# Performance work log

Measured on AMD Instinct MI355X. Metric: run time of the kernel, lower is better.

The kernel has to match this reference:

```python
import jax, jax.numpy as jnp
import numpy as np

B, L, D, H, K = 8, 2048, 1024, 16, 31
D_CONV = D // H  # 64
EPS = 1e-6


def setup_inputs() -> dict:
    key = jax.random.key(0)
    ks = jax.random.split(key, 5)
    return {
        "x": jax.random.normal(ks[0], (B, L, D), dtype=jnp.float32),
        "W_pe": (jax.random.normal(ks[1], (D_CONV, 2 * K), dtype=jnp.float32) * 0.1),
        "b_pe": jnp.zeros((2 * K,), dtype=jnp.float32),
        "stt_energy": jnp.ones((1, H, 1, K), dtype=jnp.float32)
                      + 0.02 * jax.random.normal(ks[2], (1, H, 1, K), dtype=jnp.float32),
        "W_fc": jax.random.normal(ks[3], (D, D), dtype=jnp.float32) / jnp.sqrt(jnp.float32(D)),
        "gamma": jnp.ones((D,), dtype=jnp.float32),
        "beta": jnp.zeros((D,), dtype=jnp.float32),
    }


def reference(x, W_pe, b_pe, stt_energy, W_fc, gamma, beta):
    b, l, d_model = x.shape
    d = d_model // H
    residual = x

    # mask_table matmul == causal running mean: avg[t] = mean(x[0..t])
    avg = jnp.cumsum(x, axis=1) / jnp.arange(1, l + 1, dtype=x.dtype)[None, :, None]

    # (B, L, H, d) -> (B*H, L, d)
    ci = avg.reshape(b, l, H, d).transpose(0, 2, 1, 3).reshape(b * H, l, d)

    pc = ci @ W_pe + b_pe                      # (BH, L, 2K)
    dyn, gate = pc[..., :K], pc[..., K:]
    stt = jnp.broadcast_to(stt_energy, (b, H, 1, K)).reshape(b * H, 1, K)
    energy = stt + jax.nn.sigmoid(gate) * dyn  # (BH, L, K)

    # as_strided banded softmax: energy[t,k] attends position t+k-(K-1);
    # -10000 fillers underflow to 0 in fp32, and out-of-range (negative position)
    # weights are dropped WITHOUT renormalization, as in the original slicing.
    w = jax.nn.softmax(energy, axis=-1)        # (BH, L, K)
    t_idx = jnp.arange(l)[:, None]
    k_idx = jnp.arange(K)[None, :]
    w = jnp.where(t_idx + k_idx - (K - 1) >= 0, w, jnp.zeros((), x.dtype))

    # banded bmm: out[t] = sum_k w[t,k] * ci[t+k-(K-1)]
    padded = jnp.pad(ci, ((0, 0), (K - 1, 0), (0, 0)))  # (BH, L+K-1, d)
    out = jnp.zeros((b * H, l, d), dtype=x.dtype)
    for kk in range(K):  # small fixed kernel-size loop
        out = out + w[:, :, kk:kk + 1] * padded[:, kk:kk + l, :]

    conv_loc = out.reshape(b, H, l, d).transpose(0, 2, 1, 3).reshape(b, l, d_model)

    v = conv_loc @ W_fc.T + residual
    mu = jnp.mean(v, axis=-1, keepdims=True)
    var = jnp.var(v, axis=-1, keepdims=True)
    v = (v - mu) / jnp.sqrt(var + EPS) * gamma + beta
    return v
```

## Files before the change

kernel.cpp:

```cpp
#include <hip/hip_runtime.h>
#include <math.h>

#define BB 8
#define LL 2048
#define DD 1024
#define HH 16
#define DH 64
#define KK 31
#define NSEG 32
#define SEGLEN 64

#define TLEN 64
#define TROW 2080
#define TSTR2 112
#define WBSTR2 104
#define WPESTR2 72
#define PCSS 64

typedef __attribute__((ext_vector_type(8))) short bf16x8;
typedef __attribute__((ext_vector_type(4))) float f32x4;
typedef __attribute__((ext_vector_type(8))) unsigned short u16x8;

__device__ __forceinline__ unsigned short f2bf(float f) {
    unsigned u = __float_as_uint(f);
    unsigned r = (u + 0x7fffu + ((u >> 16) & 1u)) >> 16;
    return (unsigned short)r;
}
__device__ __forceinline__ float bf2f(unsigned short s) {
    return __uint_as_float(((unsigned)s) << 16);
}

__device__ __forceinline__ void gload_lds16(const void* g, void* l) {
    __builtin_amdgcn_global_load_lds(
        (const __attribute__((address_space(1))) void*)g,
        (__attribute__((address_space(3))) void*)l, 16, 0, 0);
}

__global__ __launch_bounds__(256)
void seg_sum_kernel(const float* __restrict__ x, float* __restrict__ segsum) {
    int g = blockIdx.x * 256 + threadIdx.x;
    int d = g & (DD - 1);
    int s = (g >> 10) & (NSEG - 1);
    int b = g >> 15;
    const float* p = x + (size_t)(b * LL + s * SEGLEN) * DD + d;
    float acc = 0.f;
    #pragma unroll 8
    for (int i = 0; i < SEGLEN; ++i) acc += p[(size_t)i * DD];
    segsum[g] = acc;
}

__global__ __launch_bounds__(256)
void avg_kernel(const float* __restrict__ x, const float* __restrict__ segsum,
                unsigned short* __restrict__ avgT) {
    int g = blockIdx.x * 256 + threadIdx.x;
    int d = g & (DD - 1);
    int s = (g >> 10) & (NSEG - 1);
    int b = g >> 15;
    float run = 0.f;
    const float* ss = segsum + ((size_t)b << 15) + d;
    for (int s2 = 0; s2 < s; ++s2) run += ss[s2 << 10];
    const float* p = x + (size_t)(b * LL + s * SEGLEN) * DD + d;
    unsigned short* rowt = avgT +
        ((size_t)(b * HH + (d >> 6)) * DH + (d & 63)) * TROW;
    unsigned short* qt = rowt + 32 + s * SEGLEN;
    if (s == 0) {
        u16x8 z = {};
        #pragma unroll
        for (int j = 0; j < 4; ++j) *(u16x8*)&rowt[j * 8] = z;
    }
    int t0 = s * SEGLEN;
    #pragma unroll
    for (int j = 0; j < 8; ++j) {
        u16x8 v;
        #pragma unroll
        for (int e = 0; e < 8; ++e) {
            int i = j * 8 + e;
            run += p[(size_t)i * DD];
            v[e] = f2bf(run / (float)(t0 + i + 1));
        }
        *(u16x8*)&qt[j * 8] = v;
    }
}

__global__ __launch_bounds__(256, 4)
void conv_kernel(const unsigned short* __restrict__ avgT,
                 const unsigned short* __restrict__ wpeT,
                 const float* __restrict__ b_pe, const float* __restrict__ stt,
                 unsigned short* __restrict__ conv) {
    __shared__ __align__(16) unsigned short pcs[64 * PCSS];
    __shared__ __align__(16) unsigned short winT[64 * TSTR2];
    __shared__ __align__(16) unsigned short wub[64 * WBSTR2];

    int tid = threadIdx.x;
    int tile = blockIdx.x & 31;
    int bh = blockIdx.x >> 5;
    int b = bh >> 4, h = bh & 15;
    int t0 = tile * TLEN;
    int wv = tid >> 6, ln = tid & 63;
    int g = ln >> 4, li = ln & 15;

    {
        const unsigned short* gT = avgT + (size_t)(b * HH + h) * DH * TROW;
        #pragma unroll
        for (int q = 0; q < 3; ++q) {
            int i = tid + q * 256;
            int d = i / 14, c = i - d * 14;
            gload_lds16(gT + (size_t)d * TROW + t0 + c * 8, winT + (i & ~63) * 8);
        }
        if (tid < 128) {
            int i = 768 + tid;
            int d = i / 14, c = i - d * 14;
            gload_lds16(gT + (size_t)d * TROW + t0 + c * 8, winT + (i & ~63) * 8);
        }
        #pragma unroll
        for (int q = 0; q < 2; ++q) {
            int i = tid + q * 256;
            gload_lds16(wpeT + i * 8, wub + (i & ~63) * 8);
        }
        if (tid < 64) {
            int i = 512 + tid;
            gload_lds16(wpeT + i * 8, wub + (i & ~63) * 8);
        }
    }
    __syncthreads();

    f32x4 pacc[4];
    {
        int q32 = 32 + wv * 16 + li;
        bf16x8 a0, a1;
        #pragma unroll
        for (int e = 0; e < 8; ++e) {
            a0[e] = (short)winT[(g * 8 + e) * TSTR2 + q32];
            a1[e] = (short)winT[(32 + g * 8 + e) * TSTR2 + q32];
        }
        #pragma unroll
        for (int n = 0; n < 4; ++n) {
            int c = n * 16 + li;
            bf16x8 b0 = *(const bf16x8*)&wub[c * WPESTR2 + g * 8];
            bf16x8 b1 = *(const bf16x8*)&wub[c * WPESTR2 + 32 + g * 8];
            f32x4 z = {0.f, 0.f, 0.f, 0.f};
            z = __builtin_amdgcn_mfma_f32_16x16x32_bf16(a0, b0, z, 0, 0, 0);
            z = __builtin_amdgcn_mfma_f32_16x16x32_bf16(a1, b1, z, 0, 0, 0);
            pacc[n] = z;
        }
    }
    __syncthreads();

    {
        #pragma unroll
        for (int n = 0; n < 4; ++n) {
            int c = n * 16 + li;
            float bp = (c < 2 * KK) ? b_pe[c] : 0.f;
            #pragma unroll
            for (int r = 0; r < 4; ++r)
                pcs[(wv * 16 + g * 4 + r) * PCSS + c] = f2bf(pacc[n][r] + bp);
        }
        for (int i = tid; i < 64 * WBSTR2 / 8; i += 256) {
            u16x8 z = {};
            *(u16x8*)&wub[i * 8] = z;
        }
    }
    __syncthreads();

    {
        int half = ln >> 5, k = ln & 31;
        int kc = (k < KK) ? k : 0;
        float sttk = stt[h * KK + kc];
        for (int it = 0; it < 8; ++it) {
            int tok = wv * 16 + it * 2 + half;
            float dyn  = bf2f(pcs[tok * PCSS + kc]);
            float gate = bf2f(pcs[tok * PCSS + KK + kc]);
            float e = 0.f;
            if (k < KK) e = __expf(sttk + dyn / (1.f + __expf(-gate)));
            float sum = e;
            #pragma unroll
            for (int off = 16; off; off >>= 1) sum += __shfl_xor(sum, off, 64);
            float wvl = e / sum;
            if (k < KK && t0 + tok + k >= KK - 1)
                wub[tok * WBSTR2 + tok + k + 2] = f2bf(wvl);
        }
    }
    __syncthreads();

    {
        int row = wv * 16 + li;
        bf16x8 wa0 = *(const bf16x8*)&wub[row * WBSTR2 + g * 8];
        bf16x8 wa1 = *(const bf16x8*)&wub[row * WBSTR2 + 32 + g * 8];
        bf16x8 wa2 = *(const bf16x8*)&wub[row * WBSTR2 + 64 + g * 8];
        f32x4 cacc[4];
        #pragma unroll
        for (int n = 0; n < 4; ++n) {
            int c = n * 16 + li;
            bf16x8 b0 = *(const bf16x8*)&winT[c * TSTR2 + g * 8];
            bf16x8 b1 = *(const bf16x8*)&winT[c * TSTR2 + 32 + g * 8];
            bf16x8 b2 = *(const bf16x8*)&winT[c * TSTR2 + 64 + g * 8];
            f32x4 z = {0.f, 0.f, 0.f, 0.f};
            z = __builtin_amdgcn_mfma_f32_16x16x32_bf16(wa0, b0, z, 0, 0, 0);
            z = __builtin_amdgcn_mfma_f32_16x16x32_bf16(wa1, b1, z, 0, 0, 0);
            z = __builtin_amdgcn_mfma_f32_16x16x32_bf16(wa2, b2, z, 0, 0, 0);
            cacc[n] = z;
        }
        #pragma unroll
        for (int n = 0; n < 4; ++n)
            #pragma unroll
            for (int r = 0; r < 4; ++r)
                pcs[(wv * 16 + g * 4 + r) * PCSS + n * 16 + li] =
                    f2bf(cacc[n][r]);
    }
    __syncthreads();

    {
        int tok = tid >> 2, j0 = (tid & 3) * 16;
        u16x8 v0 = *(const u16x8*)&pcs[tok * PCSS + j0];
        u16x8 v1 = *(const u16x8*)&pcs[tok * PCSS + j0 + 8];
        unsigned short* o = conv + (size_t)(b * LL + t0 + tok) * DD + h * DH + j0;
        *(u16x8*)&o[0] = v0;
        *(u16x8*)&o[8] = v1;
    }
}

__global__ __launch_bounds__(256)
void cvt_kernel(const float* __restrict__ in, unsigned short* __restrict__ out,
                const float* __restrict__ W_pe, unsigned short* __restrict__ wpeT) {
    if (blockIdx.x == 1024) {
        for (int i = threadIdx.x; i < 64 * WPESTR2; i += 256) {
            int c = i / WPESTR2, d = i - c * WPESTR2;
            float v = (c < 2 * KK && d < 64) ? W_pe[d * (2 * KK) + c] : 0.f;
            wpeT[i] = f2bf(v);
        }
        return;
    }
    int i = (blockIdx.x * 256 + threadIdx.x) * 4;
    float4 v = *(const float4*)&in[i];
    ushort4 o;
    o.x = f2bf(v.x); o.y = f2bf(v.y); o.z = f2bf(v.z); o.w = f2bf(v.w);
    *(ushort4*)&out[i] = o;
}

#define WAITV2() do { asm volatile("s_waitcnt vmcnt(2)" ::: "memory"); \
                      __builtin_amdgcn_sched_barrier(0); } while (0)
#define WAITV0() do { asm volatile("s_waitcnt vmcnt(0)" ::: "memory"); \
                      __builtin_amdgcn_sched_barrier(0); } while (0)
#define BAR()    do { __builtin_amdgcn_s_barrier(); \
                      __builtin_amdgcn_sched_barrier(0); } while (0)

__global__ __launch_bounds__(512, 2)
void gemm_mfma_kernel(const unsigned short* __restrict__ A,
                      const unsigned short* __restrict__ Bt,
                      const float* __restrict__ X,
                      unsigned short* __restrict__ Vb)
{
    __shared__ __align__(16) unsigned short As0[256 * 64];
    __shared__ __align__(16) unsigned short Bs0[256 * 64];
    __shared__ __align__(16) unsigned short As1[256 * 64];
    __shared__ __align__(16) unsigned short Bs1[256 * 64];
    int tid = threadIdx.x;
    int wv = tid >> 6, ln = tid & 63;
    int bid = blockIdx.x;
    int nbid = (bid & 7) * 32 + (bid >> 3);
    int bm0 = (nbid >> 2) * 256;
    int bn0 = (nbid & 3) * 256;
    int wr = wv >> 2, wc = wv & 3;

    const unsigned short* ga[4];
    const unsigned short* gb[4];
    int ldo[4];
    #pragma unroll
    for (int i = 0; i < 4; ++i) {
        int dci = i * 512 + wv * 64 + ln;
        int row = dci >> 3, ch = dci & 7;
        int sc = ch ^ (row & 7);
        ga[i] = A  + (size_t)(bm0 + row) * 1024 + sc * 8;
        gb[i] = Bt + (size_t)(bn0 + row) * 1024 + sc * 8;
        ldo[i] = dci * 8;
    }

    f32x4 acc[8][4] = {};
    int la = wr * 128 + (ln & 15);
    int lb = wc * 64 + (ln & 15);
    int kg = ln >> 4;

#define TILE(RA, RB, SA, SB, ktn, LAST)                                       \
  {                                                                           \
    if (!(LAST)) { gload_lds16(ga[0] + (ktn), SA + ldo[0]);                   \
                   gload_lds16(ga[1] + (ktn), SA + ldo[1]); }                 \
    if (LAST) { WAITV0(); } else { WAITV2(); }                                \
    BAR();                                                                    \
    bf16x8 bfr[4][2];                                                         \
    _Pragma("unroll")                                                         \
    for (int n = 0; n < 4; ++n)                                               \
      _Pragma("unroll")                                                       \
      for (int ks = 0; ks < 2; ++ks) {                                        \
        int row = lb + n * 16;                                                \
        bfr[n][ks] = *(const bf16x8*)&RB[row * 64 +                           \
                        (((kg + ks * 4) ^ (row & 7)) * 8)];                   \
      }                                                                       \
    _Pragma("unroll")                                                         \
    for (int mq = 0; mq < 4; ++mq) {                                          \
      if (!(LAST)) {                                                          \
        if (mq == 1) { gload_lds16(ga[2] + (ktn), SA + ldo[2]);               \
                       gload_lds16(ga[3] + (ktn), SA + ldo[3]); }             \
        if (mq == 2) { gload_lds16(gb[0] + (ktn), SB + ldo[0]);               \
                       gload_lds16(gb[1] + (ktn), SB + ldo[1]); }             \
        if (mq == 3) { gload_lds16(gb[2] + (ktn), SB + ldo[2]);               \
                       gload_lds16(gb[3] + (ktn), SB + ldo[3]); }             \
      }                                                                       \
      bf16x8 af[2][2];                                                        \
      _Pragma("unroll")                                                       \
      for (int mm = 0; mm < 2; ++mm)                                          \
        _Pragma("unroll")                                                     \
        for (int ks = 0; ks < 2; ++ks) {                                      \
          int row = la + (mq * 2 + mm) * 16;                                  \
          af[mm][ks] = *(const bf16x8*)&RA[row * 64 +                         \
                          (((kg + ks * 4) ^ (row & 7)) * 8)];                 \
        }                                                                     \
      __builtin_amdgcn_s_setprio(1);                                          \
      _Pragma("unroll")                                                       \
      for (int mm = 0; mm < 2; ++mm)                                          \
        _Pragma("unroll")                                                     \
        for (int n = 0; n < 4; ++n)                                           \
          _Pragma("unroll")                                                   \
          for (int ks = 0; ks < 2; ++ks)                                      \
            acc[mq * 2 + mm][n] = __builtin_amdgcn_mfma_f32_16x16x32_bf16(    \
                af[mm][ks], bfr[n][ks], acc[mq * 2 + mm][n], 0, 0, 0);        \
      __builtin_amdgcn_s_setprio(0);                                          \
    }                                                                         \
    BAR();                                                                    \
  }

    #pragma unroll
    for (int i = 0; i < 4; ++i) {
        gload_lds16(ga[i], As0 + ldo[i]);
        gload_lds16(gb[i], Bs0 + ldo[i]);
    }
    for (int t2 = 0; t2 < 7; ++t2) {
        int k0 = t2 * 128;
        TILE(As0, Bs0, As1, Bs1, k0 + 64, 0);
        TILE(As1, Bs1, As0, Bs0, k0 + 128, 0);
    }
    TILE(As0, Bs0, As1, Bs1, 15 * 64, 0);
    TILE(As1, Bs1, As0, Bs0, 0, 1);
#undef TILE

    int rb0 = bm0 + wr * 128 + (ln >> 4) * 4;
    int cb0 = bn0 + wc * 64 + (ln & 15);
    #pragma unroll
    for (int m = 0; m < 8; ++m) {
        #pragma unroll
        for (int r = 0; r < 4; ++r) {
            int row = rb0 + m * 16 + r;
            size_t off = (size_t)row * 1024 + cb0;
            #pragma unroll
            for (int n = 0; n < 4; ++n)
                Vb[off + n * 16] = f2bf(acc[m][n][r] + X[off + n * 16]);
        }
    }
}

__global__ __launch_bounds__(256)
void ln_kernel(const unsigned short* __restrict__ Vb,
               const float* __restrict__ gamma,
               const float* __restrict__ beta,
               float* __restrict__ out) {
    __shared__ float red[8];
    int row = blockIdx.x;
    int tid = threadIdx.x;
    ushort4 vu = *(const ushort4*)&Vb[(size_t)row * 1024 + tid * 4];
    float v0 = bf2f(vu.x), v1 = bf2f(vu.y), v2 = bf2f(vu.z), v3 = bf2f(vu.w);
    float s = v0 + v1 + v2 + v3;
    float s2 = v0 * v0 + v1 * v1 + v2 * v2 + v3 * v3;
    #pragma unroll
    for (int off = 32; off; off >>= 1) {
        s  += __shfl_xor(s, off, 64);
        s2 += __shfl_xor(s2, off, 64);
    }
    if ((tid & 63) == 0) { red[(tid >> 6) * 2] = s; red[(tid >> 6) * 2 + 1] = s2; }
    __syncthreads();
    s  = red[0] + red[2] + red[4] + red[6];
    s2 = red[1] + red[3] + red[5] + red[7];
    float mu = s * (1.f / 1024.f);
    float var = s2 * (1.f / 1024.f) - mu * mu;
    float rs = rsqrtf(var + 1e-6f);
    float4 g  = *(const float4*)&gamma[tid * 4];
    float4 be = *(const float4*)&beta[tid * 4];
    float4 o = make_float4((v0 - mu) * rs * g.x + be.x,
                           (v1 - mu) * rs * g.y + be.y,
                           (v2 - mu) * rs * g.z + be.z,
                           (v3 - mu) * rs * g.w + be.w);
    *(float4*)&out[(size_t)row * 1024 + tid * 4] = o;
}

extern "C" void kernel_launch(void* const* d_in, const int* in_sizes, int n_in,
                              void* d_out, int out_size, void* d_ws, size_t ws_size,
                              hipStream_t stream) {
    const float* x     = (const float*)d_in[0];
    const float* W_pe  = (const float*)d_in[1];
    const float* b_pe  = (const float*)d_in[2];
    const float* stt   = (const float*)d_in[3];
    const float* W_fc  = (const float*)d_in[4];
    const float* gamma = (const float*)d_in[5];
    const float* beta  = (const float*)d_in[6];
    float* out = (float*)d_out;

    char* ws = (char*)d_ws;
    unsigned short* Vb    = (unsigned short*)ws;
    unsigned short* avgT  = (unsigned short*)(ws + (size_t)32 * 1024 * 1024);
    unsigned short* convb = (unsigned short*)(ws + (size_t)68 * 1024 * 1024);
    unsigned short* wfcb  = (unsigned short*)(ws + (size_t)100 * 1024 * 1024);
    unsigned short* wpeT  = (unsigned short*)(ws + (size_t)102 * 1024 * 1024);
    float*          segs  = (float*)(ws + (size_t)103 * 1024 * 1024);

    seg_sum_kernel<<<1024, 256, 0, stream>>>(x, segs);
    avg_kernel<<<1024, 256, 0, stream>>>(x, segs, avgT);
    cvt_kernel<<<1025, 256, 0, stream>>>(W_fc, wfcb, W_pe, wpeT);
    conv_kernel<<<4096, 256, 0, stream>>>(avgT, wpeT, b_pe, stt, convb);
    gemm_mfma_kernel<<<256, 512, 0, stream>>>(convb, wfcb, x, Vb);
    ln_kernel<<<16384, 256, 0, stream>>>(Vb, gamma, beta, out);
}
```

Before: 147.5 us.

## Restructure GEMM main loop into barrier-phased LDS-read/MFMA schedule

Replaces the macro-unrolled double-buffered GEMM tile with a rolled loop split into four phases. Each phase reads LDS fragments, issues part of the next tile's global-to-LDS loads, then hits a barrier and waits on lgkmcnt before its MFMA burst. The aim is to keep waves in lockstep so LDS reads and MFMA execution are separated cleanly and global loads overlap compute. It adds many more workgroup barriers per tile and now waits for all vector memory before the last phase, which could add stalls.

```diff
diff --git a/kernel.cpp b/kernel.cpp
--- a/kernel.cpp
+++ b/kernel.cpp
@@ -237,11 +237,12 @@
     *(ushort4*)&out[i] = o;
 }
 
-#define WAITV2() do { asm volatile("s_waitcnt vmcnt(2)" ::: "memory"); \
-                      __builtin_amdgcn_sched_barrier(0); } while (0)
 #define WAITV0() do { asm volatile("s_waitcnt vmcnt(0)" ::: "memory"); \
                       __builtin_amdgcn_sched_barrier(0); } while (0)
-#define BAR()    do { __builtin_amdgcn_s_barrier(); \
+#define LGK0()   do { asm volatile("s_waitcnt lgkmcnt(0)" ::: "memory"); \
+                      __builtin_amdgcn_sched_barrier(0); } while (0)
+#define BAR()    do { __builtin_amdgcn_sched_barrier(0); \
+                      __builtin_amdgcn_s_barrier(); \
                       __builtin_amdgcn_sched_barrier(0); } while (0)
 
 __global__ __launch_bounds__(512, 2)
@@ -280,13 +281,7 @@
     int lb = wc * 64 + (ln & 15);
     int kg = ln >> 4;
 
-#define TILE(RA, RB, SA, SB, ktn, LAST)                                       \
-  {                                                                           \
-    if (!(LAST)) { gload_lds16(ga[0] + (ktn), SA + ldo[0]);                   \
-                   gload_lds16(ga[1] + (ktn), SA + ldo[1]); }                 \
-    if (LAST) { WAITV0(); } else { WAITV2(); }                                \
-    BAR();                                                                    \
-    bf16x8 bfr[4][2];                                                         \
+#define READ_BFR(RB)                                                          \
     _Pragma("unroll")                                                         \
     for (int n = 0; n < 4; ++n)                                               \
       _Pragma("unroll")                                                       \
@@ -294,53 +289,74 @@
         int row = lb + n * 16;                                                \
         bfr[n][ks] = *(const bf16x8*)&RB[row * 64 +                           \
                         (((kg + ks * 4) ^ (row & 7)) * 8)];                   \
-      }                                                                       \
+      }
+
+#define READ_AF(RA, MQ)                                                       \
     _Pragma("unroll")                                                         \
-    for (int mq = 0; mq < 4; ++mq) {                                          \
-      if (!(LAST)) {                                                          \
-        if (mq == 1) { gload_lds16(ga[2] + (ktn), SA + ldo[2]);               \
-                       gload_lds16(ga[3] + (ktn), SA + ldo[3]); }             \
-        if (mq == 2) { gload_lds16(gb[0] + (ktn), SB + ldo[0]);               \
-                       gload_lds16(gb[1] + (ktn), SB + ldo[1]); }             \
-        if (mq == 3) { gload_lds16(gb[2] + (ktn), SB + ldo[2]);               \
-                       gload_lds16(gb[3] + (ktn), SB + ldo[3]); }             \
-      }                                                                       \
-      bf16x8 af[2][2];                                                        \
+    for (int mm = 0; mm < 2; ++mm)                                            \
       _Pragma("unroll")                                                       \
-      for (int mm = 0; mm < 2; ++mm)                                          \
+      for (int ks = 0; ks < 2; ++ks) {                                        \
+        int row = la + ((MQ) * 2 + mm) * 16;                                  \
+        af[mm][ks] = *(const bf16x8*)&RA[row * 64 +                           \
+                        (((kg + ks * 4) ^ (row & 7)) * 8)];                   \
+      }
+
+#define MFMAQ(MQ)                                                             \
+    __builtin_amdgcn_s_setprio(1);                                            \
+    _Pragma("unroll")                                                         \
+    for (int mm = 0; mm < 2; ++mm)                                            \
+      _Pragma("unroll")                                                       \
+      for (int n = 0; n < 4; ++n)                                             \
         _Pragma("unroll")                                                     \
-        for (int ks = 0; ks < 2; ++ks) {                                      \
-          int row = la + (mq * 2 + mm) * 16;                                  \
-          af[mm][ks] = *(const bf16x8*)&RA[row * 64 +                         \
-                          (((kg + ks * 4) ^ (row & 7)) * 8)];                 \
-        }                                                                     \
-      __builtin_amdgcn_s_setprio(1);                                          \
-      _Pragma("unroll")                                                       \
-      for (int mm = 0; mm < 2; ++mm)                                          \
-        _Pragma("unroll")                                                     \
-        for (int n = 0; n < 4; ++n)                                           \
-          _Pragma("unroll")                                                   \
-          for (int ks = 0; ks < 2; ++ks)                                      \
-            acc[mq * 2 + mm][n] = __builtin_amdgcn_mfma_f32_16x16x32_bf16(    \
-                af[mm][ks], bfr[n][ks], acc[mq * 2 + mm][n], 0, 0, 0);        \
-      __builtin_amdgcn_s_setprio(0);                                          \
-    }                                                                         \
-    BAR();                                                                    \
-  }
+        for (int ks = 0; ks < 2; ++ks)                                        \
+          acc[(MQ) * 2 + mm][n] = __builtin_amdgcn_mfma_f32_16x16x32_bf16(    \
+              af[mm][ks], bfr[n][ks], acc[(MQ) * 2 + mm][n], 0, 0, 0);        \
+    __builtin_amdgcn_s_setprio(0);
 
     #pragma unroll
     for (int i = 0; i < 4; ++i) {
         gload_lds16(ga[i], As0 + ldo[i]);
         gload_lds16(gb[i], Bs0 + ldo[i]);
     }
-    for (int t2 = 0; t2 < 7; ++t2) {
-        int k0 = t2 * 128;
-        TILE(As0, Bs0, As1, Bs1, k0 + 64, 0);
-        TILE(As1, Bs1, As0, Bs0, k0 + 128, 0);
-    }
-    TILE(As0, Bs0, As1, Bs1, 15 * 64, 0);
-    TILE(As1, Bs1, As0, Bs0, 0, 1);
-#undef TILE
+    WAITV0(); BAR();
+
+    unsigned short* Ac = As0; unsigned short* Bc = Bs0;
+    unsigned short* An = As1; unsigned short* Bn = Bs1;
+    for (int t = 0; t < 16; ++t) {
+        int ktn = (t + 1) * 64;
+        bool last = (t == 15);
+        bf16x8 bfr[4][2], af[2][2];
+        READ_BFR(Bc); READ_AF(Ac, 0);
+        if (!last) { gload_lds16(ga[0] + ktn, An + ldo[0]);
+                     gload_lds16(ga[1] + ktn, An + ldo[1]);
+                     gload_lds16(gb[0] + ktn, Bn + ldo[0]);
+                     gload_lds16(gb[1] + ktn, Bn + ldo[1]); }
+        BAR(); LGK0();
+        MFMAQ(0);
+        BAR();
+        READ_AF(Ac, 1);
+        if (!last) { gload_lds16(ga[2] + ktn, An + ldo[2]);
+                     gload_lds16(ga[3] + ktn, An + ldo[3]);
+                     gload_lds16(gb[2] + ktn, Bn + ldo[2]);
+                     gload_lds16(gb[3] + ktn, Bn + ldo[3]); }
+        BAR(); LGK0();
+        MFMAQ(1);
+        BAR();
+        READ_AF(Ac, 2);
+        BAR(); LGK0();
+        MFMAQ(2);
+        BAR();
+        READ_AF(Ac, 3);
+        if (!last) WAITV0();
+        BAR(); LGK0();
+        MFMAQ(3);
+        BAR();
+        unsigned short* tA = Ac; Ac = An; An = tA;
+        unsigned short* tB = Bc; Bc = Bn; Bn = tB;
+    }
+#undef READ_BFR
+#undef READ_AF
+#undef MFMAQ
 
     int rb0 = bm0 + wr * 128 + (ln >> 4) * 4;
     int cb0 = bn0 + wc * 64 + (ln & 15);
```

New measurement: 147.5 us. About the same (+0.0%).
